# Kernel tuning notes

Measured on AMD Instinct MI355X. Metric: run time of the kernel, lower is better.

## Reference

```python
import jax, jax.numpy as jnp
import numpy as np

N = 262144
C_IN = 256
C_OUT = 256
B = C_OUT // 4  # bottleneck width = 64
K = 27          # 3x3x3 kernel offsets
EPS = 1e-5


def bn(x, gamma, beta):
    # BatchNorm (training mode): per-channel stats over all points, biased var
    m = jnp.mean(x, axis=0)
    v = jnp.var(x, axis=0)
    return (x - m) * jax.lax.rsqrt(v + EPS) * gamma + beta


def sparse_conv3(x, idx_kn, W):
    # x: [N, B]; idx_kn: [K, N] neighbor index per offset; W: [K, B, B]
    # gather-GEMM-accumulate per kernel offset (avoids [N, K, B] blowup)
    def step(acc, kw):
        ik, Wk = kw
        return acc + x[ik] @ Wk, None
    acc0 = jnp.zeros((x.shape[0], W.shape[2]), x.dtype)
    acc, _ = jax.lax.scan(step, acc0, (idx_kn, W))
    return acc


def setup_inputs() -> dict:
    key = jax.random.key(0)
    ks = jax.random.split(key, 12)
    x = jax.random.normal(ks[0], (N, C_IN), dtype=jnp.float32)
    neighbor_idx = jax.random.randint(ks[1], (N, K), 0, N, dtype=jnp.int32)
    s1 = np.float32(np.sqrt(2.0 / C_IN))
    s3 = np.float32(np.sqrt(2.0 / (K * B)))
    s2 = np.float32(np.sqrt(2.0 / B))
    return {
        "x": x,
        "neighbor_idx": neighbor_idx,
        "W1a": jax.random.normal(ks[2], (C_IN, B), dtype=jnp.float32) * s1,
        "g1a": jnp.ones((B,), jnp.float32),
        "b1a": jnp.zeros((B,), jnp.float32),
        "W3": jax.random.normal(ks[3], (K, B, B), dtype=jnp.float32) * s3,
        "g3": jnp.ones((B,), jnp.float32),
        "b3": jnp.zeros((B,), jnp.float32),
        "W1b": jax.random.normal(ks[4], (B, C_OUT), dtype=jnp.float32) * s2,
        "g1b": jnp.ones((C_OUT,), jnp.float32),
        "b1b": jnp.zeros((C_OUT,), jnp.float32),
    }


def reference(x, neighbor_idx, W1a, g1a, b1a, W3, g3, b3, W1b, g1b, b1b):
    # conv1x1a: 1x1 sparse conv == per-point matmul, then BN + ReLU
    h = jax.nn.relu(bn(x @ W1a, g1a, b1a))
    # conv3x3: gather-GEMM-scatter over 27 offsets, then BN + ReLU
    h = jax.nn.relu(bn(sparse_conv3(h, neighbor_idx.T, W3), g3, b3))
    # conv1x1b: expansion, BN (no ReLU)
    h = bn(h @ W1b, g1b, b1b)
    # in_channels == out_channels -> conv1x1c is None, residual is x
    return jax.nn.relu(h + x)
```

## Files before the change

### kernel.cpp

```cpp
#include <hip/hip_runtime.h>
#include <stdint.h>

#define NPTS 262144
#define KOFF 27
#define EPS 1e-5f

typedef __attribute__((ext_vector_type(8))) short short8;
typedef __attribute__((ext_vector_type(4))) float floatx4;

__device__ __forceinline__ floatx4 mfma16(short8 a, short8 b, floatx4 c) {
    return __builtin_amdgcn_mfma_f32_16x16x32_bf16(a, b, c, 0, 0, 0);
}

__device__ __forceinline__ uint16_t f2bf(float f) {
    union { float f; uint32_t u; } v; v.f = f;
    return (uint16_t)((v.u + 0x7FFFu + ((v.u >> 16) & 1u)) >> 16);
}

__global__ void k_prep(const float* __restrict__ W1a, const float* __restrict__ W3,
                       const float* __restrict__ W1b, uint16_t* __restrict__ w1aT,
                       uint16_t* __restrict__ w3T, uint16_t* __restrict__ w1bT,
                       float* __restrict__ stats) {
    int t = blockIdx.x * 256 + threadIdx.x;
    int stride = gridDim.x * 256;
    for (int i = t; i < 64 * 256; i += stride) {
        int n = i >> 8, k = i & 255;
        w1aT[i] = f2bf(W1a[k * 64 + n]);
    }
    for (int i = t; i < KOFF * 64 * 64; i += stride) {
        int kk = i >> 12; int r = i & 4095; int o = r >> 6; int in_ = r & 63;
        w3T[i] = f2bf(W3[kk * 4096 + in_ * 64 + o]);
    }
    for (int i = t; i < 256 * 64; i += stride) {
        int n = i >> 6, k = i & 63;
        w1bT[i] = f2bf(W1b[k * 256 + n]);
    }
    for (int i = t; i < 64 * 768; i += stride) stats[i] = 0.f;
}

__global__ __launch_bounds__(256) void k_gemm1(const float* __restrict__ x,
        const uint16_t* __restrict__ w1aT, float* __restrict__ y,
        float* __restrict__ stats) {
    __shared__ uint16_t xs[64 * 264];
    __shared__ float ssum[64], ssq[64];
    const int t = threadIdx.x;
    const int base = blockIdx.x * 64;
    const float4* xv = (const float4*)(x + (size_t)base * 256);
#pragma unroll
    for (int i = 0; i < 16; ++i) {
        int f = t + 256 * i;
        int r = f >> 6, c4 = f & 63;
        float4 v = xv[f];
        uint32_t lo = (uint32_t)f2bf(v.x) | ((uint32_t)f2bf(v.y) << 16);
        uint32_t hi = (uint32_t)f2bf(v.z) | ((uint32_t)f2bf(v.w) << 16);
        uint32_t* dst = (uint32_t*)&xs[r * 264 + c4 * 4];
        dst[0] = lo; dst[1] = hi;
    }
    if (t < 64) { ssum[t] = 0.f; ssq[t] = 0.f; }
    __syncthreads();
    const int wave = t >> 6, lane = t & 63;
    const int m = lane & 15, quad = lane >> 4;
    floatx4 zero = {0.f, 0.f, 0.f, 0.f};
    floatx4 acc[4] = {zero, zero, zero, zero};
    const uint16_t* arow = &xs[(wave * 16 + m) * 264 + quad * 8];
#pragma unroll
    for (int ks = 0; ks < 8; ++ks) {
        short8 a = *(const short8*)(arow + ks * 32);
#pragma unroll
        for (int nf = 0; nf < 4; ++nf) {
            short8 b = *(const short8*)(w1aT + (nf * 16 + m) * 256 + ks * 32 + quad * 8);
            acc[nf] = mfma16(a, b, acc[nf]);
        }
    }
    const int bank = blockIdx.x & 63;
    float* sb = stats + bank * 768;
#pragma unroll
    for (int nf = 0; nf < 4; ++nf) {
        float s = 0.f, q = 0.f;
#pragma unroll
        for (int r = 0; r < 4; ++r) {
            float v = acc[nf][r];
            int pt = base + wave * 16 + quad * 4 + r;
            y[(size_t)pt * 64 + nf * 16 + m] = v;
            s += v; q += v * v;
        }
        s += __shfl_xor(s, 16); q += __shfl_xor(q, 16);
        s += __shfl_xor(s, 32); q += __shfl_xor(q, 32);
        if (quad == 0) { atomicAdd(&ssum[nf * 16 + m], s); atomicAdd(&ssq[nf * 16 + m], q); }
    }
    __syncthreads();
    if (t < 64) { atomicAdd(&sb[t], ssum[t]); atomicAdd(&sb[64 + t], ssq[t]); }
}

__global__ void k_fin(const float* __restrict__ stats, const float* __restrict__ g,
                      const float* __restrict__ bta, float* __restrict__ consts,
                      int nch, int soff, int coff) {
    int c = blockIdx.x * blockDim.x + threadIdx.x;
    if (c >= nch) return;
    float s = 0.f, q = 0.f;
    for (int b = 0; b < 64; ++b) {
        s += stats[b * 768 + soff + c];
        q += stats[b * 768 + soff + nch + c];
    }
    float mean = s / (float)NPTS;
    float var = q / (float)NPTS - mean * mean;
    float sc = g[c] * rsqrtf(var + EPS);
    consts[coff + c] = sc;
    consts[coff + nch + c] = bta[c] - mean * sc;
}

__global__ __launch_bounds__(256) void k_bnrelu(const float* __restrict__ y,
        const float* __restrict__ consts, uint16_t* __restrict__ h) {
    int t = blockIdx.x * 256 + threadIdx.x;
    size_t off = (size_t)t * 8;
    float4 v0 = *(const float4*)(y + off);
    float4 v1 = *(const float4*)(y + off + 4);
    int cbase = (int)(off & 63);
    float vs[8] = {v0.x, v0.y, v0.z, v0.w, v1.x, v1.y, v1.z, v1.w};
    union { uint16_t u[8]; uint4 v; } r;
#pragma unroll
    for (int i = 0; i < 8; ++i) {
        int c = cbase + i;
        float u = vs[i] * consts[c] + consts[64 + c];
        r.u[i] = f2bf(u > 0.f ? u : 0.f);
    }
    *(uint4*)(h + off) = r.v;
}

__global__ __launch_bounds__(256) void k_conv3(const uint16_t* __restrict__ h,
        const int* __restrict__ nidx, const uint16_t* __restrict__ w3T,
        float* __restrict__ y, float* __restrict__ stats) {
    __shared__ uint16_t as_[64 * 72];
    __shared__ uint16_t bs[64 * 72];
    __shared__ int idxs[64 * 27];
    __shared__ float ssum[64], ssq[64];
    const int t = threadIdx.x;
    const int base = blockIdx.x * 64;
    for (int i = t; i < 64 * 27; i += 256) idxs[i] = nidx[(size_t)base * 27 + i];
    if (t < 64) { ssum[t] = 0.f; ssq[t] = 0.f; }
    const int wave = t >> 6, lane = t & 63;
    const int m = lane & 15, quad = lane >> 4;
    const int gp = t >> 2, gq = (t & 3) * 16;
    floatx4 zero = {0.f, 0.f, 0.f, 0.f};
    floatx4 acc[4] = {zero, zero, zero, zero};
    __syncthreads();
    for (int k = 0; k < KOFF; ++k) {
        const uint4* wsrc = (const uint4*)(w3T + k * 4096);
        uint4 w0 = wsrc[t];
        uint4 w1 = wsrc[t + 256];
        int grow = idxs[gp * 27 + k];
        const uint4* gsrc = (const uint4*)(h + (size_t)grow * 64);
        uint4 g0 = gsrc[(t & 3) * 2];
        uint4 g1 = gsrc[(t & 3) * 2 + 1];
        *(uint4*)&bs[(t >> 3) * 72 + (t & 7) * 8] = w0;
        *(uint4*)&bs[((t >> 3) + 32) * 72 + (t & 7) * 8] = w1;
        *(uint4*)&as_[gp * 72 + gq] = g0;
        *(uint4*)&as_[gp * 72 + gq + 8] = g1;
        __syncthreads();
        const uint16_t* arow = &as_[(wave * 16 + m) * 72 + quad * 8];
#pragma unroll
        for (int ks = 0; ks < 2; ++ks) {
            short8 a = *(const short8*)(arow + ks * 32);
#pragma unroll
            for (int nf = 0; nf < 4; ++nf) {
                short8 b = *(const short8*)&bs[(nf * 16 + m) * 72 + ks * 32 + quad * 8];
                acc[nf] = mfma16(a, b, acc[nf]);
            }
        }
        __syncthreads();
    }
    const int bank = blockIdx.x & 63;
    float* sb = stats + bank * 768;
#pragma unroll
    for (int nf = 0; nf < 4; ++nf) {
        float s = 0.f, q = 0.f;
#pragma unroll
        for (int r = 0; r < 4; ++r) {
            float v = acc[nf][r];
            int pt = base + wave * 16 + quad * 4 + r;
            y[(size_t)pt * 64 + nf * 16 + m] = v;
            s += v; q += v * v;
        }
        s += __shfl_xor(s, 16); q += __shfl_xor(q, 16);
        s += __shfl_xor(s, 32); q += __shfl_xor(q, 32);
        if (quad == 0) { atomicAdd(&ssum[nf * 16 + m], s); atomicAdd(&ssq[nf * 16 + m], q); }
    }
    __syncthreads();
    if (t < 64) { atomicAdd(&sb[128 + t], ssum[t]); atomicAdd(&sb[192 + t], ssq[t]); }
}

__global__ __launch_bounds__(256) void k_gemm3(const float* __restrict__ y,
        const float* __restrict__ consts, const uint16_t* __restrict__ w1bT,
        uint16_t* __restrict__ h2, float* __restrict__ stats) {
    __shared__ uint16_t as_[64 * 72];
    __shared__ uint16_t bs[256 * 72];
    __shared__ float ssum[256], ssq[256];
    __shared__ float cf[128];
    const int t = threadIdx.x;
    const int base = blockIdx.x * 64;
    if (t < 128) cf[t] = consts[128 + t];
    ssum[t] = 0.f; ssq[t] = 0.f;
    const uint4* wsrc = (const uint4*)w1bT;
#pragma unroll
    for (int i = 0; i < 8; ++i) {
        int c = t + 256 * i;
        uint4 v = wsrc[c];
        *(uint4*)&bs[(c >> 3) * 72 + (c & 7) * 8] = v;
    }
    __syncthreads();
    const int r = t >> 2, cb = (t & 3) * 16;
    const float4* ysrc = (const float4*)(y + (size_t)(base + r) * 64 + cb);
    union { uint16_t u[16]; uint4 v[2]; } tmp;
#pragma unroll
    for (int j = 0; j < 4; ++j) {
        float4 v = ysrc[j];
        float vv[4] = {v.x, v.y, v.z, v.w};
#pragma unroll
        for (int e = 0; e < 4; ++e) {
            int c = cb + j * 4 + e;
            float u = vv[e] * cf[c] + cf[64 + c];
            tmp.u[j * 4 + e] = f2bf(u > 0.f ? u : 0.f);
        }
    }
    *(uint4*)&as_[r * 72 + cb] = tmp.v[0];
    *(uint4*)&as_[r * 72 + cb + 8] = tmp.v[1];
    *(uint4*)(h2 + (size_t)(base + r) * 64 + cb) = tmp.v[0];
    *(uint4*)(h2 + (size_t)(base + r) * 64 + cb + 8) = tmp.v[1];
    __syncthreads();
    const int wave = t >> 6, lane = t & 63;
    const int m = lane & 15, quad = lane >> 4;
    floatx4 zero = {0.f, 0.f, 0.f, 0.f};
    floatx4 acc[16];
#pragma unroll
    for (int i = 0; i < 16; ++i) acc[i] = zero;
    const uint16_t* arow = &as_[(wave * 16 + m) * 72 + quad * 8];
#pragma unroll
    for (int ks = 0; ks < 2; ++ks) {
        short8 a = *(const short8*)(arow + ks * 32);
#pragma unroll
        for (int nf = 0; nf < 16; ++nf) {
            short8 b = *(const short8*)&bs[(nf * 16 + m) * 72 + ks * 32 + quad * 8];
            acc[nf] = mfma16(a, b, acc[nf]);
        }
    }
    const int bank = blockIdx.x & 63;
#pragma unroll
    for (int nf = 0; nf < 16; ++nf) {
        float s = 0.f, q = 0.f;
#pragma unroll
        for (int rr = 0; rr < 4; ++rr) { float v = acc[nf][rr]; s += v; q += v * v; }
        s += __shfl_xor(s, 16); q += __shfl_xor(q, 16);
        s += __shfl_xor(s, 32); q += __shfl_xor(q, 32);
        if (quad == 0) { atomicAdd(&ssum[nf * 16 + m], s); atomicAdd(&ssq[nf * 16 + m], q); }
    }
    __syncthreads();
    atomicAdd(&stats[bank * 768 + 256 + t], ssum[t]);
    atomicAdd(&stats[bank * 768 + 512 + t], ssq[t]);
}

__global__ __launch_bounds__(256) void k_final(const uint16_t* __restrict__ h2,
        const uint16_t* __restrict__ w1bT, const float* __restrict__ consts,
        const float* __restrict__ x, float* __restrict__ out) {
    __shared__ uint16_t as_[64 * 72];
    __shared__ uint16_t bs[256 * 72];
    const int t = threadIdx.x;
    const int base = blockIdx.x * 64;
    const uint4* wsrc = (const uint4*)w1bT;
#pragma unroll
    for (int i = 0; i < 8; ++i) {
        int c = t + 256 * i;
        uint4 v = wsrc[c];
        *(uint4*)&bs[(c >> 3) * 72 + (c & 7) * 8] = v;
    }
    const uint4* hsrc = (const uint4*)(h2 + (size_t)base * 64);
#pragma unroll
    for (int i = 0; i < 2; ++i) {
        int c = t + 256 * i;
        uint4 v = hsrc[c];
        *(uint4*)&as_[(c >> 3) * 72 + (c & 7) * 8] = v;
    }
    __syncthreads();
    const int wave = t >> 6, lane = t & 63;
    const int m = lane & 15, quad = lane >> 4;
    floatx4 zero = {0.f, 0.f, 0.f, 0.f};
    floatx4 acc[16];
#pragma unroll
    for (int i = 0; i < 16; ++i) acc[i] = zero;
    const uint16_t* arow = &as_[(wave * 16 + m) * 72 + quad * 8];
#pragma unroll
    for (int ks = 0; ks < 2; ++ks) {
        short8 a = *(const short8*)(arow + ks * 32);
#pragma unroll
        for (int nf = 0; nf < 16; ++nf) {
            short8 b = *(const short8*)&bs[(nf * 16 + m) * 72 + ks * 32 + quad * 8];
            acc[nf] = mfma16(a, b, acc[nf]);
        }
    }
#pragma unroll
    for (int nf = 0; nf < 16; ++nf) {
        int ch = nf * 16 + m;
        float sc = consts[256 + ch], sh = consts[512 + ch];
#pragma unroll
        for (int r = 0; r < 4; ++r) {
            int pt = base + wave * 16 + quad * 4 + r;
            size_t o = (size_t)pt * 256 + ch;
            float v = acc[nf][r] * sc + sh + x[o];
            out[o] = v > 0.f ? v : 0.f;
        }
    }
}

extern "C" void kernel_launch(void* const* d_in, const int* in_sizes, int n_in,
                              void* d_out, int out_size, void* d_ws, size_t ws_size,
                              hipStream_t stream) {
    const float* x   = (const float*)d_in[0];
    const int* nidx  = (const int*)d_in[1];
    const float* W1a = (const float*)d_in[2];
    const float* g1a = (const float*)d_in[3];
    const float* b1a = (const float*)d_in[4];
    const float* W3  = (const float*)d_in[5];
    const float* g3  = (const float*)d_in[6];
    const float* b3  = (const float*)d_in[7];
    const float* W1b = (const float*)d_in[8];
    const float* g1b = (const float*)d_in[9];
    const float* b1b = (const float*)d_in[10];
    float* out = (float*)d_out;

    float* y = (float*)d_ws;
    uint16_t* h = (uint16_t*)(y + (size_t)NPTS * 64);
    uint16_t* w1aT = h + (size_t)NPTS * 64;
    uint16_t* w3T  = w1aT + 64 * 256;
    uint16_t* w1bT = w3T + KOFF * 64 * 64;
    float* stats  = (float*)(w1bT + 256 * 64);
    float* consts = stats + 64 * 768;

    k_prep<<<64, 256, 0, stream>>>(W1a, W3, W1b, w1aT, w3T, w1bT, stats);
    k_gemm1<<<NPTS / 64, 256, 0, stream>>>(x, w1aT, y, stats);
    k_fin<<<1, 64, 0, stream>>>(stats, g1a, b1a, consts, 64, 0, 0);
    k_bnrelu<<<NPTS * 64 / (256 * 8), 256, 0, stream>>>(y, consts, h);
    k_conv3<<<NPTS / 64, 256, 0, stream>>>(h, nidx, w3T, y, stats);
    k_fin<<<1, 64, 0, stream>>>(stats, g3, b3, consts, 64, 128, 128);
    k_gemm3<<<NPTS / 64, 256, 0, stream>>>(y, consts, w1bT, h, stats);
    k_fin<<<1, 256, 0, stream>>>(stats, g1b, b1b, consts, 256, 256, 256);
    k_final<<<NPTS / 64, 256, 0, stream>>>(h, w1bT, consts, x, out);
}
```

Measured before the change: 813.7 us.

## Retile sparse conv with register prefetch, swizzled LDS, bf16 intermediates, transposed indices

Measured after the change: 1.078 ms. +32.5%, slower.

```diff
diff --git a/kernel.cpp b/kernel.cpp
--- a/kernel.cpp
+++ b/kernel.cpp
@@ -15,6 +15,10 @@
 __device__ __forceinline__ uint16_t f2bf(float f) {
     union { float f; uint32_t u; } v; v.f = f;
     return (uint16_t)((v.u + 0x7FFFu + ((v.u >> 16) & 1u)) >> 16);
+}
+
+__device__ __forceinline__ float bf2f(uint16_t b) {
+    union { uint32_t u; float f; } v; v.u = ((uint32_t)b) << 16; return v.f;
 }
 
 __global__ void k_prep(const float* __restrict__ W1a, const float* __restrict__ W3,
@@ -38,8 +42,21 @@
     for (int i = t; i < 64 * 768; i += stride) stats[i] = 0.f;
 }
 
+__global__ __launch_bounds__(256) void k_tidx(const int* __restrict__ nidx,
+                                              int* __restrict__ idxT) {
+    __shared__ int s[256 * KOFF];
+    const int t = threadIdx.x;
+    const size_t base = (size_t)blockIdx.x * 256;
+    const int* src = nidx + base * KOFF;
+    for (int j = t; j < 256 * KOFF; j += 256) s[j] = src[j];
+    __syncthreads();
+#pragma unroll
+    for (int k = 0; k < KOFF; ++k)
+        idxT[(size_t)k * NPTS + base + t] = s[t * KOFF + k];
+}
+
 __global__ __launch_bounds__(256) void k_gemm1(const float* __restrict__ x,
-        const uint16_t* __restrict__ w1aT, float* __restrict__ y,
+        const uint16_t* __restrict__ w1aT, uint16_t* __restrict__ ybf,
         float* __restrict__ stats) {
     __shared__ uint16_t xs[64 * 264];
     __shared__ float ssum[64], ssq[64];
@@ -73,23 +90,44 @@
         }
     }
     const int bank = blockIdx.x & 63;
-    float* sb = stats + bank * 768;
 #pragma unroll
     for (int nf = 0; nf < 4; ++nf) {
         float s = 0.f, q = 0.f;
 #pragma unroll
         for (int r = 0; r < 4; ++r) {
             float v = acc[nf][r];
-            int pt = base + wave * 16 + quad * 4 + r;
-            y[(size_t)pt * 64 + nf * 16 + m] = v;
             s += v; q += v * v;
         }
         s += __shfl_xor(s, 16); q += __shfl_xor(q, 16);
         s += __shfl_xor(s, 32); q += __shfl_xor(q, 32);
         if (quad == 0) { atomicAdd(&ssum[nf * 16 + m], s); atomicAdd(&ssq[nf * 16 + m], q); }
     }
-    __syncthreads();
-    if (t < 64) { atomicAdd(&sb[t], ssum[t]); atomicAdd(&sb[64 + t], ssq[t]); }
+#pragma unroll
+    for (int nf = 0; nf < 4; ++nf) {
+#pragma unroll
+        for (int r = 0; r < 4; ++r) {
+            float v = acc[nf][r];
+            float pv = __shfl_xor(v, 1);
+            if ((lane & 1) == 0) {
+                int pt = wave * 16 + quad * 4 + r;
+                int ch = nf * 16 + m;
+                uint32_t pk = (uint32_t)f2bf(v) | ((uint32_t)f2bf(pv) << 16);
+                *(uint32_t*)&xs[pt * 264 + ch] = pk;
+            }
+        }
+    }
+    __syncthreads();
+    if (t < 64) {
+        float* sb = stats + bank * 768;
+        atomicAdd(&sb[t], ssum[t]); atomicAdd(&sb[64 + t], ssq[t]);
+    }
+#pragma unroll
+    for (int i = 0; i < 2; ++i) {
+        int G = t + 256 * i;
+        int row = G >> 3, g = G & 7;
+        uint4 v = *(const uint4*)&xs[row * 264 + g * 8];
+        *(uint4*)(ybf + ((size_t)(base + row)) * 64 + g * 8) = v;
+    }
 }
 
 __global__ void k_fin(const float* __restrict__ stats, const float* __restrict__ g,
@@ -109,87 +147,124 @@
     consts[coff + nch + c] = bta[c] - mean * sc;
 }
 
-__global__ __launch_bounds__(256) void k_bnrelu(const float* __restrict__ y,
-        const float* __restrict__ consts, uint16_t* __restrict__ h) {
-    int t = blockIdx.x * 256 + threadIdx.x;
-    size_t off = (size_t)t * 8;
-    float4 v0 = *(const float4*)(y + off);
-    float4 v1 = *(const float4*)(y + off + 4);
-    int cbase = (int)(off & 63);
-    float vs[8] = {v0.x, v0.y, v0.z, v0.w, v1.x, v1.y, v1.z, v1.w};
-    union { uint16_t u[8]; uint4 v; } r;
-#pragma unroll
-    for (int i = 0; i < 8; ++i) {
-        int c = cbase + i;
-        float u = vs[i] * consts[c] + consts[64 + c];
-        r.u[i] = f2bf(u > 0.f ? u : 0.f);
-    }
-    *(uint4*)(h + off) = r.v;
-}
-
-__global__ __launch_bounds__(256) void k_conv3(const uint16_t* __restrict__ h,
-        const int* __restrict__ nidx, const uint16_t* __restrict__ w3T,
-        float* __restrict__ y, float* __restrict__ stats) {
-    __shared__ uint16_t as_[64 * 72];
-    __shared__ uint16_t bs[64 * 72];
-    __shared__ int idxs[64 * 27];
+__global__ __launch_bounds__(256) void k_bnrelu(const uint16_t* __restrict__ ybf,
+        const float* __restrict__ consts, uint16_t* __restrict__ h1) {
+    __shared__ float cf[128];
+    const int t = threadIdx.x;
+    if (t < 128) cf[t] = consts[t];
+    __syncthreads();
+    size_t off = ((size_t)blockIdx.x * 256 + t) * 8;
+    uint4 v = *(const uint4*)(ybf + off);
+    int cb = (int)(off & 63);
+    uint32_t w[4] = {v.x, v.y, v.z, v.w};
+    union { uint16_t u[8]; uint4 q; } r;
+#pragma unroll
+    for (int i = 0; i < 4; ++i) {
+        float f0 = bf2f((uint16_t)(w[i] & 0xffffu));
+        float f1 = bf2f((uint16_t)(w[i] >> 16));
+        int c = cb + i * 2;
+        float u0 = f0 * cf[c] + cf[64 + c];
+        float u1 = f1 * cf[c + 1] + cf[64 + c + 1];
+        r.u[i * 2]     = f2bf(u0 > 0.f ? u0 : 0.f);
+        r.u[i * 2 + 1] = f2bf(u1 > 0.f ? u1 : 0.f);
+    }
+    *(uint4*)(h1 + off) = r.q;
+}
+
+__global__ __launch_bounds__(256, 3) void k_conv3(const uint16_t* __restrict__ h1,
+        const int* __restrict__ idxT, const uint16_t* __restrict__ w3T,
+        uint16_t* __restrict__ y2, float* __restrict__ stats) {
+    __shared__ uint16_t as_[256 * 64];
+    __shared__ uint16_t bs[64 * 64];
     __shared__ float ssum[64], ssq[64];
     const int t = threadIdx.x;
-    const int base = blockIdx.x * 64;
-    for (int i = t; i < 64 * 27; i += 256) idxs[i] = nidx[(size_t)base * 27 + i];
+    const int base = blockIdx.x * 256;
     if (t < 64) { ssum[t] = 0.f; ssq[t] = 0.f; }
     const int wave = t >> 6, lane = t & 63;
     const int m = lane & 15, quad = lane >> 4;
-    const int gp = t >> 2, gq = (t & 3) * 16;
-    floatx4 zero = {0.f, 0.f, 0.f, 0.f};
-    floatx4 acc[4] = {zero, zero, zero, zero};
-    __syncthreads();
+    const int sx = m & 7;
+    floatx4 acc[4][4];
+#pragma unroll
+    for (int a = 0; a < 4; ++a)
+#pragma unroll
+        for (int b = 0; b < 4; ++b) acc[a][b] = (floatx4){0.f, 0.f, 0.f, 0.f};
+    uint4 ga[8], wb0, wb1;
+    {
+        int gi = idxT[base + t];
+        const uint4* gs = (const uint4*)(h1 + (size_t)gi * 64);
+#pragma unroll
+        for (int g = 0; g < 8; ++g) ga[g] = gs[g];
+        const uint4* ws = (const uint4*)w3T;
+        wb0 = ws[t]; wb1 = ws[t + 256];
+    }
+    char* asb = (char*)as_;
+    char* bsb = (char*)bs;
+    const int tx = t & 7;
     for (int k = 0; k < KOFF; ++k) {
-        const uint4* wsrc = (const uint4*)(w3T + k * 4096);
-        uint4 w0 = wsrc[t];
-        uint4 w1 = wsrc[t + 256];
-        int grow = idxs[gp * 27 + k];
-        const uint4* gsrc = (const uint4*)(h + (size_t)grow * 64);
-        uint4 g0 = gsrc[(t & 3) * 2];
-        uint4 g1 = gsrc[(t & 3) * 2 + 1];
-        *(uint4*)&bs[(t >> 3) * 72 + (t & 7) * 8] = w0;
-        *(uint4*)&bs[((t >> 3) + 32) * 72 + (t & 7) * 8] = w1;
-        *(uint4*)&as_[gp * 72 + gq] = g0;
-        *(uint4*)&as_[gp * 72 + gq + 8] = g1;
         __syncthreads();
-        const uint16_t* arow = &as_[(wave * 16 + m) * 72 + quad * 8];
+#pragma unroll
+        for (int g = 0; g < 8; ++g)
+            *(uint4*)(asb + t * 128 + ((g ^ tx) << 4)) = ga[g];
+        {
+            int r0 = t >> 3;
+            *(uint4*)(bsb + r0 * 128 + ((tx ^ (r0 & 7)) << 4)) = wb0;
+            int r1 = (t + 256) >> 3;
+            *(uint4*)(bsb + r1 * 128 + ((tx ^ (r1 & 7)) << 4)) = wb1;
+        }
+        __syncthreads();
+        if (k + 1 < KOFF) {
+            int gi = idxT[(size_t)(k + 1) * NPTS + base + t];
+            const uint4* gs = (const uint4*)(h1 + (size_t)gi * 64);
+#pragma unroll
+            for (int g = 0; g < 8; ++g) ga[g] = gs[g];
+            const uint4* ws = (const uint4*)(w3T + (k + 1) * 4096);
+            wb0 = ws[t]; wb1 = ws[t + 256];
+        }
 #pragma unroll
         for (int ks = 0; ks < 2; ++ks) {
-            short8 a = *(const short8*)(arow + ks * 32);
+            int gq = ks * 4 + quad;
+            short8 bfr[4];
 #pragma unroll
             for (int nf = 0; nf < 4; ++nf) {
-                short8 b = *(const short8*)&bs[(nf * 16 + m) * 72 + ks * 32 + quad * 8];
-                acc[nf] = mfma16(a, b, acc[nf]);
+                int rn = nf * 16 + m;
+                bfr[nf] = *(const short8*)(bsb + rn * 128 + ((gq ^ sx) << 4));
             }
-        }
-        __syncthreads();
+#pragma unroll
+            for (int mt = 0; mt < 4; ++mt) {
+                int r = wave * 64 + mt * 16 + m;
+                short8 a = *(const short8*)(asb + r * 128 + ((gq ^ sx) << 4));
+#pragma unroll
+                for (int nf = 0; nf < 4; ++nf)
+                    acc[mt][nf] = mfma16(a, bfr[nf], acc[mt][nf]);
+            }
+        }
     }
     const int bank = blockIdx.x & 63;
-    float* sb = stats + bank * 768;
 #pragma unroll
     for (int nf = 0; nf < 4; ++nf) {
         float s = 0.f, q = 0.f;
 #pragma unroll
-        for (int r = 0; r < 4; ++r) {
-            float v = acc[nf][r];
-            int pt = base + wave * 16 + quad * 4 + r;
-            y[(size_t)pt * 64 + nf * 16 + m] = v;
-            s += v; q += v * v;
+        for (int mt = 0; mt < 4; ++mt) {
+#pragma unroll
+            for (int r = 0; r < 4; ++r) {
+                float v = acc[mt][nf][r];
+                int pt = base + wave * 64 + mt * 16 + quad * 4 + r;
+                y2[(size_t)pt * 64 + nf * 16 + m] = f2bf(v);
+                s += v; q += v * v;
+            }
         }
         s += __shfl_xor(s, 16); q += __shfl_xor(q, 16);
         s += __shfl_xor(s, 32); q += __shfl_xor(q, 32);
         if (quad == 0) { atomicAdd(&ssum[nf * 16 + m], s); atomicAdd(&ssq[nf * 16 + m], q); }
     }
     __syncthreads();
-    if (t < 64) { atomicAdd(&sb[128 + t], ssum[t]); atomicAdd(&sb[192 + t], ssq[t]); }
-}
-
-__global__ __launch_bounds__(256) void k_gemm3(const float* __restrict__ y,
+    if (t < 64) {
+        atomicAdd(&stats[bank * 768 + 128 + t], ssum[t]);
+        atomicAdd(&stats[bank * 768 + 192 + t], ssq[t]);
+    }
+}
+
+__global__ __launch_bounds__(256) void k_gemm3(const uint16_t* __restrict__ y2,
         const float* __restrict__ consts, const uint16_t* __restrict__ w1bT,
         uint16_t* __restrict__ h2, float* __restrict__ stats) {
     __shared__ uint16_t as_[64 * 72];
@@ -208,24 +283,26 @@
         *(uint4*)&bs[(c >> 3) * 72 + (c & 7) * 8] = v;
     }
     __syncthreads();
-    const int r = t >> 2, cb = (t & 3) * 16;
-    const float4* ysrc = (const float4*)(y + (size_t)(base + r) * 64 + cb);
-    union { uint16_t u[16]; uint4 v[2]; } tmp;
-#pragma unroll
-    for (int j = 0; j < 4; ++j) {
-        float4 v = ysrc[j];
-        float vv[4] = {v.x, v.y, v.z, v.w};
-#pragma unroll
-        for (int e = 0; e < 4; ++e) {
-            int c = cb + j * 4 + e;
-            float u = vv[e] * cf[c] + cf[64 + c];
-            tmp.u[j * 4 + e] = f2bf(u > 0.f ? u : 0.f);
-        }
-    }
-    *(uint4*)&as_[r * 72 + cb] = tmp.v[0];
-    *(uint4*)&as_[r * 72 + cb + 8] = tmp.v[1];
-    *(uint4*)(h2 + (size_t)(base + r) * 64 + cb) = tmp.v[0];
-    *(uint4*)(h2 + (size_t)(base + r) * 64 + cb + 8) = tmp.v[1];
+#pragma unroll
+    for (int i = 0; i < 2; ++i) {
+        int G = t + 256 * i;
+        int row = G >> 3, g = G & 7;
+        uint4 v = *(const uint4*)(y2 + (size_t)(base + row) * 64 + g * 8);
+        uint32_t w[4] = {v.x, v.y, v.z, v.w};
+        union { uint16_t u[8]; uint4 q; } r;
+#pragma unroll
+        for (int j = 0; j < 4; ++j) {
+            int c = g * 8 + j * 2;
+            float f0 = bf2f((uint16_t)(w[j] & 0xffffu));
+            float f1 = bf2f((uint16_t)(w[j] >> 16));
+            float u0 = f0 * cf[c] + cf[64 + c];
+            float u1 = f1 * cf[c + 1] + cf[64 + c + 1];
+            r.u[j * 2]     = f2bf(u0 > 0.f ? u0 : 0.f);
+            r.u[j * 2 + 1] = f2bf(u1 > 0.f ? u1 : 0.f);
+        }
+        *(uint4*)&as_[row * 72 + g * 8] = r.q;
+        *(uint4*)(h2 + (size_t)(base + row) * 64 + g * 8) = r.q;
+    }
     __syncthreads();
     const int wave = t >> 6, lane = t & 63;
     const int m = lane & 15, quad = lane >> 4;
@@ -326,21 +403,25 @@
     const float* b1b = (const float*)d_in[10];
     float* out = (float*)d_out;
 
-    float* y = (float*)d_ws;
-    uint16_t* h = (uint16_t*)(y + (size_t)NPTS * 64);
-    uint16_t* w1aT = h + (size_t)NPTS * 64;
+    uint16_t* ybf  = (uint16_t*)d_ws;
+    uint16_t* h1   = ybf + (size_t)NPTS * 64;
+    uint16_t* y2   = h1 + (size_t)NPTS * 64;
+    uint16_t* h2   = y2 + (size_t)NPTS * 64;
+    uint16_t* w1aT = h2 + (size_t)NPTS * 64;
     uint16_t* w3T  = w1aT + 64 * 256;
     uint16_t* w1bT = w3T + KOFF * 64 * 64;
-    float* stats  = (float*)(w1bT + 256 * 64);
-    float* consts = stats + 64 * 768;
+    int* idxT      = (int*)(w1bT + 256 * 64);
+    float* stats   = (float*)(idxT + (size_t)KOFF * NPTS);
+    float* consts  = stats + 64 * 768;
 
     k_prep<<<64, 256, 0, stream>>>(W1a, W3, W1b, w1aT, w3T, w1bT, stats);
-    k_gemm1<<<NPTS / 64, 256, 0, stream>>>(x, w1aT, y, stats);
+    k_tidx<<<NPTS / 256, 256, 0, stream>>>(nidx, idxT);
+    k_gemm1<<<NPTS / 64, 256, 0, stream>>>(x, w1aT, ybf, stats);
     k_fin<<<1, 64, 0, stream>>>(stats, g1a, b1a, consts, 64, 0, 0);
-    k_bnrelu<<<NPTS * 64 / (256 * 8), 256, 0, stream>>>(y, consts, h);
-    k_conv3<<<NPTS / 64, 256, 0, stream>>>(h, nidx, w3T, y, stats);
+    k_bnrelu<<<NPTS * 64 / (256 * 8), 256, 0, stream>>>(ybf, consts, h1);
+    k_conv3<<<NPTS / 256, 256, 0, stream>>>(h1, idxT, w3T, y2, stats);
     k_fin<<<1, 64, 0, stream>>>(stats, g3, b3, consts, 64, 128, 128);
-    k_gemm3<<<NPTS / 64, 256, 0, stream>>>(y, consts, w1bT, h, stats);
+    k_gemm3<<<NPTS / 64, 256, 0, stream>>>(y2, consts, w1bT, h2, stats);
     k_fin<<<1, 256, 0, stream>>>(stats, g1b, b1b, consts, 256, 256, 256);
-    k_final<<<NPTS / 64, 256, 0, stream>>>(h, w1bT, consts, x, out);
-}
+    k_final<<<NPTS / 64, 256, 0, stream>>>(h2, w1bT, consts, x, out);
+}
```
